# Kernel tuning notes

Measured on AMD Instinct MI355X. Metric: run time of the kernel, lower is better.

## Reference

```python
import jax, jax.numpy as jnp
import numpy as np

B, S, H = 32768, 16, 16  # batch, seq_len, G_hiddensize (code requires H == S and H == latent_dim == 16)
LATENT = 16
DISC_DIMS = [(1, 32), (32, 16), (16, 8), (8, 16), (16, 32)]


def setup_inputs() -> dict:
    key = jax.random.key(0)
    ks = iter(jax.random.split(key, 64))
    def p(shape, scale=0.1):
        return (jax.random.normal(next(ks), shape, dtype=jnp.float32) * scale)
    inp = dict(
        values=jax.random.normal(next(ks), (B, S), dtype=jnp.float32),
        masks=jax.random.randint(next(ks), (B, S), 0, 2).astype(jnp.int32),
        g_fwd_Wih=p((4 * H, 1)), g_fwd_Whh=p((4 * H, H)), g_fwd_b=p((4 * H,)),
        g_bwd_Wih=p((4 * H, 1)), g_bwd_Whh=p((4 * H, H)), g_bwd_b=p((4 * H,)),
        imp_W=p((1, H)), imp_b=p((1,)),
        fc_W=p((LATENT, H)), fc_b=p((LATENT,)),
        dec_Wih=p((4 * H, LATENT)), dec_Whh=p((4 * H, H)), dec_b=p((4 * H,)),
        dec_out_W=p((1, H)), dec_out_b=p((1,)),
        disc_out_W=p((1, 32)), disc_out_b=p((1,)),
    )
    for k, (i, h) in enumerate(DISC_DIMS):
        inp[f"d_W_{k}"] = p((4 * h, i))
        inp[f"d_b_{k}"] = p((4 * h,))
    return inp


def lstm_cell(x, h, c, Wih, Whh, b):
    gates = x @ Wih.T + h @ Whh.T + b
    i, f, g, o = jnp.split(gates, 4, axis=-1)
    c = jax.nn.sigmoid(f) * c + jax.nn.sigmoid(i) * jnp.tanh(g)
    h = jax.nn.sigmoid(o) * jnp.tanh(c)
    return h, c


def _forward(values, masks, g_fwd_Wih, g_fwd_Whh, g_fwd_b, g_bwd_Wih, g_bwd_Whh, g_bwd_b,
             imp_W, imp_b, fc_W, fc_b, dec_Wih, dec_Whh, dec_b, dec_out_W, dec_out_b,
             disc_out_W, disc_out_b,
             d_W_0, d_b_0, d_W_1, d_b_1, d_W_2, d_b_2, d_W_3, d_b_3, d_W_4, d_b_4):
    dt = values.dtype
    Bsz = values.shape[0]
    x = values[:, :, None]                     # (B, S, 1)
    m = masks.astype(dt)[:, :, None]           # (B, S, 1)
    # NOTE: torch.flip along axis 2 (size 1) is a no-op, so the bwd cell sees the
    # same (un-reversed) sequence as the fwd cell -- faithfully reproduced here.
    zH = jnp.zeros((Bsz, H), dt)
    h_f, c_f = lstm_cell(jnp.full((Bsz, 1), 128.0, dt), zH, zH, g_fwd_Wih, g_fwd_Whh, g_fwd_b)
    h_b, c_b = lstm_cell(jnp.full((Bsz, 1), -128.0, dt), zH, zH, g_bwd_Wih, g_bwd_Whh, g_bwd_b)

    def gen_step(carry, xm):
        h_f, c_f, h_b, c_b = carry
        x_t, m_t = xm                          # (B,1) each
        cc_f = (1 - m_t) * x_t + m_t * (h_f @ imp_W.T + imp_b)
        cc_b = (1 - m_t) * x_t + m_t * (h_b @ imp_W.T + imp_b)
        h_f, c_f = lstm_cell(cc_f, h_f, c_f, g_fwd_Wih, g_fwd_Whh, g_fwd_b)
        h_b, c_b = lstm_cell(cc_b, h_b, c_b, g_bwd_Wih, g_bwd_Whh, g_bwd_b)
        return (h_f, c_f, h_b, c_b), None

    (h_f, c_f, h_b, c_b), _ = jax.lax.scan(
        gen_step, (h_f, c_f, h_b, c_b),
        (jnp.transpose(x, (1, 0, 2)), jnp.transpose(m, (1, 0, 2))))
    h = h_f + h_b                               # (B, H), H == S
    imputations = h.reshape(Bsz, S, 1)
    imputed = imputations * (1 - m) + x * m      # (B, S, 1)

    # Discriminator: torch calls each LSTMCell WITHOUT state every timestep, so
    # hidden/cell start at zero each call -> purely feedforward per (batch, t).
    # W_hh @ 0 == 0, so only W_ih and the combined bias matter. Vectorize over B*S.
    inp = imputed.reshape(Bsz * S, 1)
    for W, b in ((d_W_0, d_b_0), (d_W_1, d_b_1), (d_W_2, d_b_2), (d_W_3, d_b_3), (d_W_4, d_b_4)):
        gates = inp @ W.T + b
        i, f, g, o = jnp.split(gates, 4, axis=-1)
        cc = jax.nn.sigmoid(i) * jnp.tanh(g)
        inp = jax.nn.sigmoid(o) * jnp.tanh(cc)
    disc_output = (inp @ disc_out_W.T + disc_out_b).reshape(Bsz, S, 1)

    latent = h @ fc_W.T + fc_b                  # (B, 16)

    # Decoder: ignores latent values (only uses batch size); start token = 128s.
    hd = cd = jnp.zeros((Bsz, H), dt)
    hd, cd = lstm_cell(jnp.full((Bsz, LATENT), 128.0, dt), hd, cd, dec_Wih, dec_Whh, dec_b)

    def dec_step(carry, _):
        hd, cd = carry
        hd, cd = lstm_cell(cd, hd, cd, dec_Wih, dec_Whh, dec_b)
        return (hd, cd), hd @ dec_out_W.T + dec_out_b

    _, outs = jax.lax.scan(dec_step, (hd, cd), None, length=S)  # (S, B, 1)
    reconstructed = jnp.transpose(outs, (1, 0, 2))
    return imputed, disc_output, latent, reconstructed


def reference(values, masks, g_fwd_Wih, g_fwd_Whh, g_fwd_b, g_bwd_Wih, g_bwd_Whh, g_bwd_b,
              imp_W, imp_b, fc_W, fc_b, dec_Wih, dec_Whh, dec_b, dec_out_W, dec_out_b,
              disc_out_W, disc_out_b,
              d_W_0, d_b_0, d_W_1, d_b_1, d_W_2, d_b_2, d_W_3, d_b_3, d_W_4, d_b_4):
    return _forward(values, masks, g_fwd_Wih, g_fwd_Whh, g_fwd_b, g_bwd_Wih, g_bwd_Whh, g_bwd_b,
                    imp_W, imp_b, fc_W, fc_b, dec_Wih, dec_Whh, dec_b, dec_out_W, dec_out_b,
                    disc_out_W, disc_out_b,
                    d_W_0, d_b_0, d_W_1, d_b_1, d_W_2, d_b_2, d_W_3, d_b_3, d_W_4, d_b_4)
```

## Files before the change

### kernel.cpp

```cpp
#include <hip/hip_runtime.h>

#define BB 32768
#define BS (BB*16)

typedef __attribute__((ext_vector_type(8))) short bf8v;
typedef __attribute__((ext_vector_type(4))) float f4v;

#define RECO 64
#define TAB  128
#define NTAB 2049
#define HFO  8448
#define HBO  (HFO+BS)

#define PW0 0
#define PB0 96
#define PW1 192
#define PB1 1920
#define PW2 1968
#define PB2 2448
#define PW3 2472
#define PB3 3048
#define PW4 3096
#define PB4 5016
#define POW 5112
#define POB 5144
#define PN  5148

__device__ __forceinline__ float sigm(float x){
    return __builtin_amdgcn_rcpf(1.f + __expf(-x));
}
__device__ __forceinline__ float tanh_f(float x){
    return 1.f - 2.f * __builtin_amdgcn_rcpf(1.f + __expf(2.f * x));
}
__device__ __forceinline__ float dunit(float gi, float gg, float go){
    return sigm(go) * tanh_f(sigm(gi) * tanh_f(gg));
}
__device__ __forceinline__ unsigned short f2bf(float f){
    union { float f; unsigned int i; } v; v.f = f;
    unsigned int x = v.i;
    unsigned int r = x + 0x7fffu + ((x >> 16) & 1u);
    return (unsigned short)(r >> 16);
}

struct P29 { const float* p[29]; };

__device__ __forceinline__ bf8v makeB(const float* Whh, const float* Wih,
                                      int row, int quad)
{
    bf8v B = {0,0,0,0,0,0,0,0};
    if (quad < 2) {
        const float4* p = (const float4*)(Whh + row*16 + quad*8);
        float4 a0 = p[0], a1 = p[1];
        B[0]=(short)f2bf(a0.x); B[1]=(short)f2bf(a0.y);
        B[2]=(short)f2bf(a0.z); B[3]=(short)f2bf(a0.w);
        B[4]=(short)f2bf(a1.x); B[5]=(short)f2bf(a1.y);
        B[6]=(short)f2bf(a1.z); B[7]=(short)f2bf(a1.w);
    } else if (quad == 2) {
        B[0] = (short)f2bf(Wih[row]);
    }
    return B;
}

__global__ __launch_bounds__(256)
void k_lstm(P29 a, const int* __restrict__ masks, float* __restrict__ ws)
{
    __shared__ __align__(16) float smem[2624];
    int tid  = threadIdx.x;
    int lane = tid & 63;
    int wv   = tid >> 6;
    int n    = lane & 15;
    int quad = lane >> 4;
    int dir  = (int)(blockIdx.x >= 512);
    int gid0 = blockIdx.x * 64 + wv * 16;
    int b0   = gid0 & 32767;
    float* wbase = smem + wv * 656;
    float* xs    = wbase;
    int*   msI   = (int*)(wbase + 256);
    unsigned short* hbp = (unsigned short*)(wbase + 512);
    float* ccf   = wbase + 640;
    const int4* hbI = (const int4*)hbp;

    {
        size_t gbase = (size_t)b0 * 16;
        int e = lane * 4;
        float4 xv = *(const float4*)(a.p[0] + gbase + e);
        int4   mv = *(const int4*)(masks + gbase + e);
        int sm = lane >> 2;
        int st = (lane & 3) * 4;
        xs[(st+0)*16 + sm] = xv.x;  msI[(st+0)*16 + sm] = mv.x;
        xs[(st+1)*16 + sm] = xv.y;  msI[(st+1)*16 + sm] = mv.y;
        xs[(st+2)*16 + sm] = xv.z;  msI[(st+2)*16 + sm] = mv.z;
        xs[(st+3)*16 + sm] = xv.w;  msI[(st+3)*16 + sm] = mv.w;
    }
    const float* __restrict__ Wih = a.p[2 + 3*dir];
    const float* __restrict__ Whh = a.p[3 + 3*dir];
    const float* __restrict__ bia = a.p[4 + 3*dir];
    bf8v Bi = makeB(Whh, Wih, n,      quad);
    bf8v Bf = makeB(Whh, Wih, 16+n,   quad);
    bf8v Bg = makeB(Whh, Wih, 32+n,   quad);
    bf8v Bo = makeB(Whh, Wih, 48+n,   quad);
    bf8v Bp = {0,0,0,0,0,0,0,0};
    if (quad < 2) {
        const float4* p = (const float4*)(a.p[8] + quad*8);
        float4 a0 = p[0], a1 = p[1];
        Bp[0]=(short)f2bf(a0.x); Bp[1]=(short)f2bf(a0.y);
        Bp[2]=(short)f2bf(a0.z); Bp[3]=(short)f2bf(a0.w);
        Bp[4]=(short)f2bf(a1.x); Bp[5]=(short)f2bf(a1.y);
        Bp[6]=(short)f2bf(a1.z); Bp[7]=(short)f2bf(a1.w);
    }
    float impb = a.p[9][0];
    float bi_ = bia[n], bf_ = bia[16+n], bg_ = bia[32+n], bo_ = bia[48+n];
    float sgn = dir ? -128.f : 128.f;
    float c0, h0;
    {
        float gi0 = sgn*Wih[n]    + bi_;
        float gg0 = sgn*Wih[32+n] + bg_;
        float go0 = sgn*Wih[48+n] + bo_;
        c0 = sigm(gi0) * tanh_f(gg0);
        h0 = sigm(go0) * tanh_f(c0);
    }
    float c[4] = {c0, c0, c0, c0};
    float h[4];
    {
        unsigned short hb0 = f2bf(h0);
        #pragma unroll
        for (int r = 0; r < 4; r++) hbp[(quad*4+r)*16 + n] = hb0;
    }
    const f4v cz = {0.f, 0.f, 0.f, 0.f};
    const bf8v Az = {0,0,0,0,0,0,0,0};
    for (int t = 0; t < 16; t++) {
        union { int4 i4; bf8v b; } au;
        au.i4 = hbI[(n << 1) | (quad & 1)];
        bf8v A = (quad < 2) ? au.b : Az;
        f4v dimp = __builtin_amdgcn_mfma_f32_16x16x32_bf16(A, Bp, cz, 0, 0, 0);
        float4 xt4 = *(const float4*)(xs + t*16 + quad*4);
        int4   mt4 = *(const int4*)(msI + t*16 + quad*4);
        float cc0 = mt4.x ? (dimp[0] + impb) : xt4.x;
        float cc1 = mt4.y ? (dimp[1] + impb) : xt4.y;
        float cc2 = mt4.z ? (dimp[2] + impb) : xt4.z;
        float cc3 = mt4.w ? (dimp[3] + impb) : xt4.w;
        if (n == 0) {
            ccf[quad*4+0] = cc0; ccf[quad*4+1] = cc1;
            ccf[quad*4+2] = cc2; ccf[quad*4+3] = cc3;
        }
        if (quad == 2) A[0] = (short)f2bf(ccf[n]);
        f4v di = __builtin_amdgcn_mfma_f32_16x16x32_bf16(A, Bi, cz, 0, 0, 0);
        f4v df = __builtin_amdgcn_mfma_f32_16x16x32_bf16(A, Bf, cz, 0, 0, 0);
        f4v dg = __builtin_amdgcn_mfma_f32_16x16x32_bf16(A, Bg, cz, 0, 0, 0);
        f4v dO = __builtin_amdgcn_mfma_f32_16x16x32_bf16(A, Bo, cz, 0, 0, 0);
        #pragma unroll
        for (int r = 0; r < 4; r++) {
            float gi = di[r] + bi_;
            float gf = df[r] + bf_;
            float gg = dg[r] + bg_;
            float go = dO[r] + bo_;
            float cn = sigm(gf)*c[r] + sigm(gi)*tanh_f(gg);
            c[r] = cn;
            float hh = sigm(go)*tanh_f(cn);
            h[r] = hh;
            hbp[(quad*4+r)*16 + n] = f2bf(hh);
        }
    }
    float* outp = ws + HFO + (size_t)dir*BS + (size_t)b0*16;
    #pragma unroll
    for (int r = 0; r < 4; r++) outp[(quad*4+r)*16 + n] = h[r];
}

__global__ __launch_bounds__(256)
void k_tabdec(P29 a, float* __restrict__ ws)
{
    __shared__ __align__(16) float wl[PN];
    int tid = threadIdx.x;
    if (blockIdx.x < 129) {
#define STAGE(WS, BSi, h, K, padK, wdst, bdst) \
    { const float* Wp = a.p[WS]; const float* Bp2 = a.p[BSi]; \
      for (int i = tid; i < 3*(h)*(K); i += 256){ \
        int r = i/(K), k = i - r*(K); int g = r/(h), u0 = r - g*(h); \
        int sr = (g==0? u0 : (g==1? 2*(h)+u0 : 3*(h)+u0)); \
        wl[(wdst) + r*(padK) + k] = Wp[sr*(K) + k]; } \
      for (int i = tid; i < 3*(h); i += 256){ \
        int g = i/(h), u0 = i - g*(h); \
        int sr = (g==0? u0 : (g==1? 2*(h)+u0 : 3*(h)+u0)); \
        wl[(bdst) + i] = Bp2[sr]; } }
        STAGE(19, 20, 32,  1,  1, PW0, PB0)
        STAGE(21, 22, 16, 32, 36, PW1, PB1)
        STAGE(23, 24,  8, 16, 20, PW2, PB2)
        STAGE(25, 26, 16,  8, 12, PW3, PB3)
        STAGE(27, 28, 32, 16, 20, PW4, PB4)
#undef STAGE
        { const float* s = a.p[17]; for (int i = tid; i < 32; i += 256) wl[POW+i] = s[i]; }
        if (tid == 0) wl[POB] = a.p[18][0];
        __syncthreads();
        int u = tid & 15;
        int gbase = (tid & 63) & 48;
        int gid = blockIdx.x * 16 + (tid >> 4);
        const float4* w4 = (const float4*)wl;
        float xin = -8.f + (float)gid * (1.f/128.f);
        float lo = dunit(xin*wl[PW0+u]    + wl[PB0+u],
                         xin*wl[PW0+32+u] + wl[PB0+32+u],
                         xin*wl[PW0+64+u] + wl[PB0+64+u]);
        float hi = dunit(xin*wl[PW0+16+u] + wl[PB0+16+u],
                         xin*wl[PW0+48+u] + wl[PB0+48+u],
                         xin*wl[PW0+80+u] + wl[PB0+80+u]);
        float A0[32];
        #pragma unroll
        for (int k = 0; k < 16; k++) { A0[k] = __shfl(lo, gbase+k); A0[16+k] = __shfl(hi, gbase+k); }
        float gi = wl[PB1+u], gg = wl[PB1+16+u], go = wl[PB1+32+u];
        int bi_ = (PW1 + u*36)>>2, bg_ = (PW1 + (16+u)*36)>>2, bo_ = (PW1 + (32+u)*36)>>2;
        #pragma unroll
        for (int q = 0; q < 8; q++) {
            float4 wi = w4[bi_+q], wg = w4[bg_+q], wo = w4[bo_+q];
            float b0=A0[4*q], b1=A0[4*q+1], b2=A0[4*q+2], b3=A0[4*q+3];
            gi += b0*wi.x + b1*wi.y + b2*wi.z + b3*wi.w;
            gg += b0*wg.x + b1*wg.y + b2*wg.z + b3*wg.w;
            go += b0*wo.x + b1*wo.y + b2*wo.z + b3*wo.w;
        }
        float a1 = dunit(gi, gg, go);
        float A1[16];
        #pragma unroll
        for (int k = 0; k < 16; k++) A1[k] = __shfl(a1, gbase+k);
        int v = u & 7;
        gi = wl[PB2+v]; gg = wl[PB2+8+v]; go = wl[PB2+16+v];
        bi_ = (PW2 + v*20)>>2; bg_ = (PW2 + (8+v)*20)>>2; bo_ = (PW2 + (16+v)*20)>>2;
        #pragma unroll
        for (int q = 0; q < 4; q++) {
            float4 wi = w4[bi_+q], wg = w4[bg_+q], wo = w4[bo_+q];
            float b0=A1[4*q], b1=A1[4*q+1], b2=A1[4*q+2], b3=A1[4*q+3];
            gi += b0*wi.x + b1*wi.y + b2*wi.z + b3*wi.w;
            gg += b0*wg.x + b1*wg.y + b2*wg.z + b3*wg.w;
            go += b0*wo.x + b1*wo.y + b2*wo.z + b3*wo.w;
        }
        float a2 = dunit(gi, gg, go);
        float A2[8];
        #pragma unroll
        for (int k = 0; k < 8; k++) A2[k] = __shfl(a2, gbase+k);
        gi = wl[PB3+u]; gg = wl[PB3+16+u]; go = wl[PB3+32+u];
        bi_ = (PW3 + u*12)>>2; bg_ = (PW3 + (16+u)*12)>>2; bo_ = (PW3 + (32+u)*12)>>2;
        #pragma unroll
        for (int q = 0; q < 2; q++) {
            float4 wi = w4[bi_+q], wg = w4[bg_+q], wo = w4[bo_+q];
            float b0=A2[4*q], b1=A2[4*q+1], b2=A2[4*q+2], b3=A2[4*q+3];
            gi += b0*wi.x + b1*wi.y + b2*wi.z + b3*wi.w;
            gg += b0*wg.x + b1*wg.y + b2*wg.z + b3*wg.w;
            go += b0*wo.x + b1*wo.y + b2*wo.z + b3*wo.w;
        }
        float a3 = dunit(gi, gg, go);
        float A3[16];
        #pragma unroll
        for (int k = 0; k < 16; k++) A3[k] = __shfl(a3, gbase+k);
        float part;
        {
            float g0i = wl[PB4+u], g0g = wl[PB4+32+u], g0o = wl[PB4+64+u];
            float g1i = wl[PB4+16+u], g1g = wl[PB4+48+u], g1o = wl[PB4+80+u];
            int c0i = (PW4 + u*20)>>2,      c0g = (PW4 + (32+u)*20)>>2, c0o = (PW4 + (64+u)*20)>>2;
            int c1i = (PW4 + (16+u)*20)>>2, c1g = (PW4 + (48+u)*20)>>2, c1o = (PW4 + (80+u)*20)>>2;
            #pragma unroll
            for (int q = 0; q < 4; q++) {
                float b0=A3[4*q], b1=A3[4*q+1], b2=A3[4*q+2], b3=A3[4*q+3];
                float4 wi = w4[c0i+q], wg = w4[c0g+q], wo = w4[c0o+q];
                g0i += b0*wi.x + b1*wi.y + b2*wi.z + b3*wi.w;
                g0g += b0*wg.x + b1*wg.y + b2*wg.z + b3*wg.w;
                g0o += b0*wo.x + b1*wo.y + b2*wo.z + b3*wo.w;
                wi = w4[c1i+q]; wg = w4[c1g+q]; wo = w4[c1o+q];
                g1i += b0*wi.x + b1*wi.y + b2*wi.z + b3*wi.w;
                g1g += b0*wg.x + b1*wg.y + b2*wg.z + b3*wg.w;
                g1o += b0*wo.x + b1*wo.y + b2*wo.z + b3*wo.w;
            }
            part = dunit(g0i, g0g, g0o)*wl[POW+u] + dunit(g1i, g1g, g1o)*wl[POW+16+u];
        }
        part += __shfl_xor(part, 1);
        part += __shfl_xor(part, 2);
        part += __shfl_xor(part, 4);
        part += __shfl_xor(part, 8);
        if (u == 0 && gid < NTAB) ws[TAB + gid] = part + wl[POB];
        return;
    }
    {
        float* dh = wl;
        float* dc = wl + 16;
        const float* Wih = a.p[12];
        const float* Whh = a.p[13];
        const float* bb  = a.p[14];
        const float* oW  = a.p[15];
        const float* ob  = a.p[16];
        float wii[16], wff[16], wgg[16], woo[16];
        float vii[16], vff[16], vgg[16], voo[16];
        float bi_r=0, bf_r=0, bg_r=0, bo_r=0;
        if (tid < 16) {
            int uu = tid;
            #pragma unroll
            for (int k = 0; k < 16; k++) {
                wii[k]=Wih[uu*16+k];      vii[k]=Whh[uu*16+k];
                wff[k]=Wih[(16+uu)*16+k]; vff[k]=Whh[(16+uu)*16+k];
                wgg[k]=Wih[(32+uu)*16+k]; vgg[k]=Whh[(32+uu)*16+k];
                woo[k]=Wih[(48+uu)*16+k]; voo[k]=Whh[(48+uu)*16+k];
            }
            bi_r=bb[uu]; bf_r=bb[16+uu]; bg_r=bb[32+uu]; bo_r=bb[48+uu];
            float gi = bi_r, gg = bg_r, go = bo_r;
            #pragma unroll
            for (int k = 0; k < 16; k++) {
                gi += 128.f * wii[k];
                gg += 128.f * wgg[k];
                go += 128.f * woo[k];
            }
            float cd0 = sigm(gi) * tanh_f(gg);
            dc[tid] = cd0; dh[tid] = sigm(go) * tanh_f(cd0);
        }
        __syncthreads();
        for (int t = 0; t < 16; t++) {
            float rx[16], rh[16], cold = 0.f;
            if (tid < 16) {
                #pragma unroll
                for (int k = 0; k < 16; k++) { rx[k] = dc[k]; rh[k] = dh[k]; }
                cold = dc[tid];
            }
            __syncthreads();
            if (tid < 16) {
                float gi = bi_r, gf = bf_r, gg = bg_r, go = bo_r;
                #pragma unroll
                for (int k = 0; k < 16; k++) {
                    gi += rx[k]*wii[k] + rh[k]*vii[k];
                    gf += rx[k]*wff[k] + rh[k]*vff[k];
                    gg += rx[k]*wgg[k] + rh[k]*vgg[k];
                    go += rx[k]*woo[k] + rh[k]*voo[k];
                }
                float cn = sigm(gf)*cold + sigm(gi)*tanh_f(gg);
                dc[tid] = cn; dh[tid] = sigm(go)*tanh_f(cn);
            }
            __syncthreads();
            if (tid == 0) {
                float o = ob[0];
                #pragma unroll
                for (int k = 0; k < 16; k++) o += dh[k] * oW[k];
                ws[RECO + t] = o;
            }
            __syncthreads();
        }
    }
}

__global__ __launch_bounds__(256) void k_post(P29 a, const int* __restrict__ masks,
                                              const float* __restrict__ ws,
                                              float* __restrict__ out)
{
    __shared__ float tab[NTAB];
    __shared__ __align__(16) float fw[256];
    __shared__ __align__(16) float rec[16];
    __shared__ float fb[16];
    int tid = threadIdx.x;
    for (int i = tid; i < NTAB; i += 256) tab[i] = ws[TAB + i];
    fw[tid] = a.p[10][tid];
    if (tid < 16) { fb[tid] = a.p[11][tid]; rec[tid] = ws[RECO + tid]; }
    __syncthreads();
    int T = blockIdx.x * 256 + tid;
    int b = T >> 2;
    int q = T & 3;
    int tq = q * 4;
    const float4* hf4 = (const float4*)(ws + HFO + (size_t)b*16);
    const float4* hb4 = (const float4*)(ws + HBO + (size_t)b*16);
    float4 s0, s1, s2, s3;
    {
        float4 f0=hf4[0], f1=hf4[1], f2=hf4[2], f3=hf4[3];
        float4 g0=hb4[0], g1=hb4[1], g2=hb4[2], g3=hb4[3];
        s0 = make_float4(f0.x+g0.x, f0.y+g0.y, f0.z+g0.z, f0.w+g0.w);
        s1 = make_float4(f1.x+g1.x, f1.y+g1.y, f1.z+g1.z, f1.w+g1.w);
        s2 = make_float4(f2.x+g2.x, f2.y+g2.y, f2.z+g2.z, f2.w+g2.w);
        s3 = make_float4(f3.x+g3.x, f3.y+g3.y, f3.z+g3.z, f3.w+g3.w);
    }
    float4 hq = (q==0) ? s0 : (q==1) ? s1 : (q==2) ? s2 : s3;
    float4 xv = *(const float4*)(a.p[0] + (size_t)b*16 + tq);
    int4   mv = *(const int4*)(masks + (size_t)b*16 + tq);
    float impv[4];
    impv[0] = mv.x ? xv.x : hq.x;
    impv[1] = mv.y ? xv.y : hq.y;
    impv[2] = mv.z ? xv.z : hq.z;
    impv[3] = mv.w ? xv.w : hq.w;
    float latv[4];
    #pragma unroll
    for (int j = 0; j < 4; j++) {
        int t = tq + j;
        const float4* wr = (const float4*)(fw + t*16);
        float4 w0=wr[0], w1=wr[1], w2=wr[2], w3=wr[3];
        float l = fb[t];
        l += s0.x*w0.x + s0.y*w0.y + s0.z*w0.z + s0.w*w0.w;
        l += s1.x*w1.x + s1.y*w1.y + s1.z*w1.z + s1.w*w1.w;
        l += s2.x*w2.x + s2.y*w2.y + s2.z*w2.z + s2.w*w2.w;
        l += s3.x*w3.x + s3.y*w3.y + s3.z*w3.z + s3.w*w3.w;
        latv[j] = l;
    }
    float dv[4];
    #pragma unroll
    for (int j = 0; j < 4; j++) {
        float xx = fminf(fmaxf(impv[j], -8.f), 8.f);
        float f = (xx + 8.f) * 128.f;
        float fi = floorf(f);
        int i = (int)fi; i = i > NTAB-2 ? NTAB-2 : i;
        float w = f - fi;
        dv[j] = fmaf(w, tab[i+1] - tab[i], tab[i]);
    }
    float4 rv = ((const float4*)rec)[q];
    size_t eo = (size_t)b*16 + tq;
    *(float4*)(out + eo)        = make_float4(impv[0], impv[1], impv[2], impv[3]);
    *(float4*)(out + BS + eo)   = make_float4(dv[0], dv[1], dv[2], dv[3]);
    *(float4*)(out + 2*BS + eo) = make_float4(latv[0], latv[1], latv[2], latv[3]);
    *(float4*)(out + 3*BS + eo) = rv;
}

extern "C" void kernel_launch(void* const* d_in, const int* in_sizes, int n_in,
                              void* d_out, int out_size, void* d_ws, size_t ws_size,
                              hipStream_t stream)
{
    float* ws = (float*)d_ws;
    P29 a;
    for (int i = 0; i < 29; i++) a.p[i] = (const float*)d_in[i];
    const int* masks = (const int*)d_in[1];
    k_tabdec<<<130, 256, 0, stream>>>(a, ws);
    k_lstm<<<1024, 256, 0, stream>>>(a, masks, ws);
    k_post<<<(BB*4)/256, 256, 0, stream>>>(a, masks, ws, (float*)d_out);
}
```

Before: 165.9 us.

## Fuse bidirectional LSTM and post-processing into one kernel per wave

```diff
diff --git a/kernel.cpp b/kernel.cpp
--- a/kernel.cpp
+++ b/kernel.cpp
@@ -9,8 +9,6 @@
 #define RECO 64
 #define TAB  128
 #define NTAB 2049
-#define HFO  8448
-#define HBO  (HFO+BS)
 
 #define PW0 0
 #define PB0 96
@@ -62,43 +60,49 @@
 }
 
 __global__ __launch_bounds__(256)
-void k_lstm(P29 a, const int* __restrict__ masks, float* __restrict__ ws)
+void k_fused(P29 a, const int* __restrict__ masks, const float* __restrict__ ws,
+             float* __restrict__ out)
 {
-    __shared__ __align__(16) float smem[2624];
+    __shared__ __align__(16) float smem[4*784];
     int tid  = threadIdx.x;
     int lane = tid & 63;
     int wv   = tid >> 6;
     int n    = lane & 15;
     int quad = lane >> 4;
-    int dir  = (int)(blockIdx.x >= 512);
-    int gid0 = blockIdx.x * 64 + wv * 16;
-    int b0   = gid0 & 32767;
-    float* wbase = smem + wv * 656;
-    float* xs    = wbase;
-    int*   msI   = (int*)(wbase + 256);
-    unsigned short* hbp = (unsigned short*)(wbase + 512);
-    float* ccf   = wbase + 640;
+    int mydir = (quad >= 2);
+    int b0   = (blockIdx.x * 4 + wv) * 8;
+    float* W = smem + wv * 784;
+    float* xs  = W;
+    int*   msI = (int*)(W + 128);
+    unsigned short* hbp = (unsigned short*)(W + 256);
+    float* ccf = W + 384;
+    float* hsf = W + 400;
+    float* hsm = W + 656;
     const int4* hbI = (const int4*)hbp;
 
-    {
-        size_t gbase = (size_t)b0 * 16;
-        int e = lane * 4;
-        float4 xv = *(const float4*)(a.p[0] + gbase + e);
-        int4   mv = *(const int4*)(masks + gbase + e);
-        int sm = lane >> 2;
-        int st = (lane & 3) * 4;
-        xs[(st+0)*16 + sm] = xv.x;  msI[(st+0)*16 + sm] = mv.x;
-        xs[(st+1)*16 + sm] = xv.y;  msI[(st+1)*16 + sm] = mv.y;
-        xs[(st+2)*16 + sm] = xv.z;  msI[(st+2)*16 + sm] = mv.z;
-        xs[(st+3)*16 + sm] = xv.w;  msI[(st+3)*16 + sm] = mv.w;
-    }
-    const float* __restrict__ Wih = a.p[2 + 3*dir];
-    const float* __restrict__ Whh = a.p[3 + 3*dir];
-    const float* __restrict__ bia = a.p[4 + 3*dir];
-    bf8v Bi = makeB(Whh, Wih, n,      quad);
-    bf8v Bf = makeB(Whh, Wih, 16+n,   quad);
-    bf8v Bg = makeB(Whh, Wih, 32+n,   quad);
-    bf8v Bo = makeB(Whh, Wih, 48+n,   quad);
+    if (lane < 32) {
+        size_t g = (size_t)b0 * 16 + lane * 4;
+        float4 xv = *(const float4*)(a.p[0] + g);
+        int4   mv = *(const int4*)(masks + g);
+        int bl = lane >> 2;
+        int t0 = (lane & 3) * 4;
+        xs[(t0+0)*8 + bl] = xv.x;  msI[(t0+0)*8 + bl] = mv.x;
+        xs[(t0+1)*8 + bl] = xv.y;  msI[(t0+1)*8 + bl] = mv.y;
+        xs[(t0+2)*8 + bl] = xv.z;  msI[(t0+2)*8 + bl] = mv.z;
+        xs[(t0+3)*8 + bl] = xv.w;  msI[(t0+3)*8 + bl] = mv.w;
+    }
+    const float* __restrict__ WihF = a.p[2];
+    const float* __restrict__ WhhF = a.p[3];
+    const float* __restrict__ WihB = a.p[5];
+    const float* __restrict__ WhhB = a.p[6];
+    bf8v BiF = makeB(WhhF, WihF, n,    quad);
+    bf8v BfF = makeB(WhhF, WihF, 16+n, quad);
+    bf8v BgF = makeB(WhhF, WihF, 32+n, quad);
+    bf8v BoF = makeB(WhhF, WihF, 48+n, quad);
+    bf8v BiB = makeB(WhhB, WihB, n,    quad);
+    bf8v BfB = makeB(WhhB, WihB, 16+n, quad);
+    bf8v BgB = makeB(WhhB, WihB, 32+n, quad);
+    bf8v BoB = makeB(WhhB, WihB, 48+n, quad);
     bf8v Bp = {0,0,0,0,0,0,0,0};
     if (quad < 2) {
         const float4* p = (const float4*)(a.p[8] + quad*8);
@@ -109,13 +113,15 @@
         Bp[6]=(short)f2bf(a1.z); Bp[7]=(short)f2bf(a1.w);
     }
     float impb = a.p[9][0];
-    float bi_ = bia[n], bf_ = bia[16+n], bg_ = bia[32+n], bo_ = bia[48+n];
-    float sgn = dir ? -128.f : 128.f;
+    const float* biaMy = a.p[4 + 3*mydir];
+    const float* WihMy = mydir ? WihB : WihF;
+    float bi_ = biaMy[n], bf_ = biaMy[16+n], bg_ = biaMy[32+n], bo_ = biaMy[48+n];
+    float sgn = mydir ? -128.f : 128.f;
     float c0, h0;
     {
-        float gi0 = sgn*Wih[n]    + bi_;
-        float gg0 = sgn*Wih[32+n] + bg_;
-        float go0 = sgn*Wih[48+n] + bo_;
+        float gi0 = sgn*WihMy[n]    + bi_;
+        float gg0 = sgn*WihMy[32+n] + bg_;
+        float go0 = sgn*WihMy[48+n] + bo_;
         c0 = sigm(gi0) * tanh_f(gg0);
         h0 = sigm(go0) * tanh_f(c0);
     }
@@ -133,8 +139,8 @@
         au.i4 = hbI[(n << 1) | (quad & 1)];
         bf8v A = (quad < 2) ? au.b : Az;
         f4v dimp = __builtin_amdgcn_mfma_f32_16x16x32_bf16(A, Bp, cz, 0, 0, 0);
-        float4 xt4 = *(const float4*)(xs + t*16 + quad*4);
-        int4   mt4 = *(const int4*)(msI + t*16 + quad*4);
+        float4 xt4 = *(const float4*)(xs + t*8 + (quad & 1)*4);
+        int4   mt4 = *(const int4*)(msI + t*8 + (quad & 1)*4);
         float cc0 = mt4.x ? (dimp[0] + impb) : xt4.x;
         float cc1 = mt4.y ? (dimp[1] + impb) : xt4.y;
         float cc2 = mt4.z ? (dimp[2] + impb) : xt4.z;
@@ -144,16 +150,20 @@
             ccf[quad*4+2] = cc2; ccf[quad*4+3] = cc3;
         }
         if (quad == 2) A[0] = (short)f2bf(ccf[n]);
-        f4v di = __builtin_amdgcn_mfma_f32_16x16x32_bf16(A, Bi, cz, 0, 0, 0);
-        f4v df = __builtin_amdgcn_mfma_f32_16x16x32_bf16(A, Bf, cz, 0, 0, 0);
-        f4v dg = __builtin_amdgcn_mfma_f32_16x16x32_bf16(A, Bg, cz, 0, 0, 0);
-        f4v dO = __builtin_amdgcn_mfma_f32_16x16x32_bf16(A, Bo, cz, 0, 0, 0);
+        f4v diF = __builtin_amdgcn_mfma_f32_16x16x32_bf16(A, BiF, cz, 0, 0, 0);
+        f4v dfF = __builtin_amdgcn_mfma_f32_16x16x32_bf16(A, BfF, cz, 0, 0, 0);
+        f4v dgF = __builtin_amdgcn_mfma_f32_16x16x32_bf16(A, BgF, cz, 0, 0, 0);
+        f4v doF = __builtin_amdgcn_mfma_f32_16x16x32_bf16(A, BoF, cz, 0, 0, 0);
+        f4v diB = __builtin_amdgcn_mfma_f32_16x16x32_bf16(A, BiB, cz, 0, 0, 0);
+        f4v dfB = __builtin_amdgcn_mfma_f32_16x16x32_bf16(A, BfB, cz, 0, 0, 0);
+        f4v dgB = __builtin_amdgcn_mfma_f32_16x16x32_bf16(A, BgB, cz, 0, 0, 0);
+        f4v doB = __builtin_amdgcn_mfma_f32_16x16x32_bf16(A, BoB, cz, 0, 0, 0);
         #pragma unroll
         for (int r = 0; r < 4; r++) {
-            float gi = di[r] + bi_;
-            float gf = df[r] + bf_;
-            float gg = dg[r] + bg_;
-            float go = dO[r] + bo_;
+            float gi = (mydir ? diB[r] : diF[r]) + bi_;
+            float gf = (mydir ? dfB[r] : dfF[r]) + bf_;
+            float gg = (mydir ? dgB[r] : dgF[r]) + bg_;
+            float go = (mydir ? doB[r] : doF[r]) + bo_;
             float cn = sigm(gf)*c[r] + sigm(gi)*tanh_f(gg);
             c[r] = cn;
             float hh = sigm(go)*tanh_f(cn);
@@ -161,9 +171,45 @@
             hbp[(quad*4+r)*16 + n] = f2bf(hh);
         }
     }
-    float* outp = ws + HFO + (size_t)dir*BS + (size_t)b0*16;
     #pragma unroll
-    for (int r = 0; r < 4; r++) outp[(quad*4+r)*16 + n] = h[r];
+    for (int r = 0; r < 4; r++) hsf[(quad*4+r)*16 + n] = h[r];
+    if (quad < 2) {
+        #pragma unroll
+        for (int r = 0; r < 4; r++) {
+            int m = quad*4 + r;
+            hsm[m*16 + n] = hsf[m*16 + n] + hsf[(m+8)*16 + n];
+        }
+    }
+    size_t gbase = (size_t)b0 * 16;
+    #pragma unroll
+    for (int half = 0; half < 2; half++) {
+        int e = half*64 + lane;
+        int bl = e >> 4, t = e & 15;
+        float x  = xs[t*8 + bl];
+        int   mk = msI[t*8 + bl];
+        float imputed = mk ? x : hsm[e];
+        const float4* hr = (const float4*)(hsm + bl*16);
+        const float4* wr = (const float4*)(a.p[10] + t*16);
+        float4 s0=hr[0], s1=hr[1], s2=hr[2], s3=hr[3];
+        float4 w0=wr[0], w1=wr[1], w2=wr[2], w3=wr[3];
+        float lat = a.p[11][t];
+        lat += s0.x*w0.x + s0.y*w0.y + s0.z*w0.z + s0.w*w0.w;
+        lat += s1.x*w1.x + s1.y*w1.y + s1.z*w1.z + s1.w*w1.w;
+        lat += s2.x*w2.x + s2.y*w2.y + s2.z*w2.z + s2.w*w2.w;
+        lat += s3.x*w3.x + s3.y*w3.y + s3.z*w3.z + s3.w*w3.w;
+        float xx = fminf(fmaxf(imputed, -8.f), 8.f);
+        float f = (xx + 8.f) * 128.f;
+        float fi = floorf(f);
+        int i = (int)fi; i = i > NTAB-2 ? NTAB-2 : i;
+        float wgt = f - fi;
+        float t0v = ws[TAB + i], t1v = ws[TAB + i + 1];
+        float dv = fmaf(wgt, t1v - t0v, t0v);
+        float rv = ws[RECO + t];
+        out[gbase + e]        = imputed;
+        out[BS + gbase + e]   = dv;
+        out[2*BS + gbase + e] = lat;
+        out[3*BS + gbase + e] = rv;
+    }
 }
 
 __global__ __launch_bounds__(256)
@@ -339,73 +385,6 @@
     }
 }
 
-__global__ __launch_bounds__(256) void k_post(P29 a, const int* __restrict__ masks,
-                                              const float* __restrict__ ws,
-                                              float* __restrict__ out)
-{
-    __shared__ float tab[NTAB];
-    __shared__ __align__(16) float fw[256];
-    __shared__ __align__(16) float rec[16];
-    __shared__ float fb[16];
-    int tid = threadIdx.x;
-    for (int i = tid; i < NTAB; i += 256) tab[i] = ws[TAB + i];
-    fw[tid] = a.p[10][tid];
-    if (tid < 16) { fb[tid] = a.p[11][tid]; rec[tid] = ws[RECO + tid]; }
-    __syncthreads();
-    int T = blockIdx.x * 256 + tid;
-    int b = T >> 2;
-    int q = T & 3;
-    int tq = q * 4;
-    const float4* hf4 = (const float4*)(ws + HFO + (size_t)b*16);
-    const float4* hb4 = (const float4*)(ws + HBO + (size_t)b*16);
-    float4 s0, s1, s2, s3;
-    {
-        float4 f0=hf4[0], f1=hf4[1], f2=hf4[2], f3=hf4[3];
-        float4 g0=hb4[0], g1=hb4[1], g2=hb4[2], g3=hb4[3];
-        s0 = make_float4(f0.x+g0.x, f0.y+g0.y, f0.z+g0.z, f0.w+g0.w);
-        s1 = make_float4(f1.x+g1.x, f1.y+g1.y, f1.z+g1.z, f1.w+g1.w);
-        s2 = make_float4(f2.x+g2.x, f2.y+g2.y, f2.z+g2.z, f2.w+g2.w);
-        s3 = make_float4(f3.x+g3.x, f3.y+g3.y, f3.z+g3.z, f3.w+g3.w);
-    }
-    float4 hq = (q==0) ? s0 : (q==1) ? s1 : (q==2) ? s2 : s3;
-    float4 xv = *(const float4*)(a.p[0] + (size_t)b*16 + tq);
-    int4   mv = *(const int4*)(masks + (size_t)b*16 + tq);
-    float impv[4];
-    impv[0] = mv.x ? xv.x : hq.x;
-    impv[1] = mv.y ? xv.y : hq.y;
-    impv[2] = mv.z ? xv.z : hq.z;
-    impv[3] = mv.w ? xv.w : hq.w;
-    float latv[4];
-    #pragma unroll
-    for (int j = 0; j < 4; j++) {
-        int t = tq + j;
-        const float4* wr = (const float4*)(fw + t*16);
-        float4 w0=wr[0], w1=wr[1], w2=wr[2], w3=wr[3];
-        float l = fb[t];
-        l += s0.x*w0.x + s0.y*w0.y + s0.z*w0.z + s0.w*w0.w;
-        l += s1.x*w1.x + s1.y*w1.y + s1.z*w1.z + s1.w*w1.w;
-        l += s2.x*w2.x + s2.y*w2.y + s2.z*w2.z + s2.w*w2.w;
-        l += s3.x*w3.x + s3.y*w3.y + s3.z*w3.z + s3.w*w3.w;
-        latv[j] = l;
-    }
-    float dv[4];
-    #pragma unroll
-    for (int j = 0; j < 4; j++) {
-        float xx = fminf(fmaxf(impv[j], -8.f), 8.f);
-        float f = (xx + 8.f) * 128.f;
-        float fi = floorf(f);
-        int i = (int)fi; i = i > NTAB-2 ? NTAB-2 : i;
-        float w = f - fi;
-        dv[j] = fmaf(w, tab[i+1] - tab[i], tab[i]);
-    }
-    float4 rv = ((const float4*)rec)[q];
-    size_t eo = (size_t)b*16 + tq;
-    *(float4*)(out + eo)        = make_float4(impv[0], impv[1], impv[2], impv[3]);
-    *(float4*)(out + BS + eo)   = make_float4(dv[0], dv[1], dv[2], dv[3]);
-    *(float4*)(out + 2*BS + eo) = make_float4(latv[0], latv[1], latv[2], latv[3]);
-    *(float4*)(out + 3*BS + eo) = rv;
-}
-
 extern "C" void kernel_launch(void* const* d_in, const int* in_sizes, int n_in,
                               void* d_out, int out_size, void* d_ws, size_t ws_size,
                               hipStream_t stream)
@@ -415,6 +394,5 @@
     for (int i = 0; i < 29; i++) a.p[i] = (const float*)d_in[i];
     const int* masks = (const int*)d_in[1];
     k_tabdec<<<130, 256, 0, stream>>>(a, ws);
-    k_lstm<<<1024, 256, 0, stream>>>(a, masks, ws);
-    k_post<<<(BB*4)/256, 256, 0, stream>>>(a, masks, ws, (float*)d_out);
-}
+    k_fused<<<1024, 256, 0, stream>>>(a, masks, ws, (float*)d_out);
+}
```

After: 163.8 us. About the same (-1.3%).
